# Kernel optimization log

Hardware: AMD Instinct MI355X
Metric: run time of the kernel (lower is better)

Reference implementation:

```python
import jax, jax.numpy as jnp
import numpy as np

B, T, C = 2, 2048, 1024
N_HEADS = 16
HEAD_DIM = C // N_HEADS

def setup_inputs() -> dict:
    key = jax.random.key(0)
    k1, k2, k3 = jax.random.split(key, 3)
    x = jax.random.normal(k1, (B, T, C), dtype=jnp.float32)
    W_qkv = jax.random.normal(k2, (C, 3 * C), dtype=jnp.float32) * (1.0 / np.sqrt(C))
    W_out = jax.random.normal(k3, (C, C), dtype=jnp.float32) * (1.0 / np.sqrt(C))
    return {"x": x, "W_qkv": W_qkv, "W_out": W_out}

def reference(x, W_qkv, W_out):
    b, t, c = x.shape
    qkv = jnp.einsum('btc,cd->btd', x, W_qkv)  # [B,T,3C]
    q, k, v = jnp.split(qkv, 3, axis=-1)
    # [B, H, T, hd]
    q = q.reshape(b, t, N_HEADS, HEAD_DIM).transpose(0, 2, 1, 3)
    k = k.reshape(b, t, N_HEADS, HEAD_DIM).transpose(0, 2, 1, 3)
    v = v.reshape(b, t, N_HEADS, HEAD_DIM).transpose(0, 2, 1, 3)
    scale = 1.0 / jnp.sqrt(jnp.asarray(HEAD_DIM, dtype=x.dtype))
    attn = jnp.einsum('bhqd,bhkd->bhqk', q, k) * scale  # [B,H,T,T]
    causal = jnp.tril(jnp.ones((t, t), dtype=bool))
    attn = jnp.where(causal, attn, jnp.asarray(-1e9, dtype=attn.dtype))
    attn = jax.nn.softmax(attn, axis=-1)
    out = jnp.einsum('bhqk,bhkd->bhqd', attn, v)
    out = out.transpose(0, 2, 1, 3).reshape(b, t, c)
    return jnp.einsum('btc,cd->btd', out, W_out)
```

## Files before the change

### kernel.cpp

```cpp
#include <hip/hip_runtime.h>
#include <hip/hip_bf16.h>

typedef __attribute__((ext_vector_type(8))) short short8;
typedef __attribute__((ext_vector_type(4))) short bf16x4;
typedef __attribute__((ext_vector_type(4))) float floatx4;

#define T_SEQ 2048
#define NH    16
#define HD    64
#define QSCALE 0.18033688f
#define EXP2(x) __builtin_amdgcn_exp2f(x)

#define MFMA16(a, b, c) __builtin_amdgcn_mfma_f32_16x16x16bf16_1k(a, b, c, 0, 0, 0)

__device__ __forceinline__ ushort f2bf(float f) {
    union { float f; unsigned u; } un; un.f = f;
    unsigned r = un.u + 0x7fff + ((un.u >> 16) & 1);
    return (ushort)(r >> 16);
}
__device__ __forceinline__ unsigned pkbf(float a, float b) {
    __hip_bfloat162 t = __float22bfloat162_rn(float2{a, b});
    return *reinterpret_cast<unsigned*>(&t);
}

typedef const __attribute__((address_space(1))) unsigned int* gp1_t;
typedef __attribute__((address_space(3))) unsigned int* lp3_t;
__device__ __forceinline__ void gl_lds16(const ushort* g, ushort* l) {
    __builtin_amdgcn_global_load_lds((gp1_t)g, (lp3_t)l, 16, 0, 0);
}

__global__ void prep_kernel(const float* __restrict__ Wqkv, const float* __restrict__ Wout,
                            const float* __restrict__ x, ushort* __restrict__ wt_qkv,
                            ushort* __restrict__ wt_out, ushort* __restrict__ x_bf) {
    __shared__ ushort tile[32][33];
    const int bid = blockIdx.x;
    if (bid >= 4096) {
        size_t i = ((size_t)(bid - 4096) * 256 + threadIdx.x) * 8;
        float4 f0 = *(const float4*)(x + i);
        float4 f1 = *(const float4*)(x + i + 4);
        short8 v;
        v[0] = (short)f2bf(f0.x); v[1] = (short)f2bf(f0.y);
        v[2] = (short)f2bf(f0.z); v[3] = (short)f2bf(f0.w);
        v[4] = (short)f2bf(f1.x); v[5] = (short)f2bf(f1.y);
        v[6] = (short)f2bf(f1.z); v[7] = (short)f2bf(f1.w);
        *(short8*)(x_bf + i) = v;
        return;
    }
    const float* in; ushort* out; int R, C, gx, gy;
    if (bid < 3072) { in = Wqkv; out = wt_qkv; R = 1024; C = 3072; gx = bid % 96; gy = bid / 96; }
    else            { int t = bid - 3072; in = Wout; out = wt_out; R = 1024; C = 1024; gx = t & 31; gy = t >> 5; }
    const int tx = threadIdx.x & 31, ty = threadIdx.x >> 5;
    const int bx = gx * 32, by = gy * 32;
    #pragma unroll
    for (int i = ty; i < 32; i += 8)
        tile[i][tx] = f2bf(in[(size_t)(by + i) * C + bx + tx]);
    __syncthreads();
    #pragma unroll
    for (int i = ty; i < 32; i += 8)
        out[(size_t)(bx + i) * R + by + tx] = tile[tx][i];
}

template <int EPI>
__global__ __launch_bounds__(256, 3)
void gemm_bt(const ushort* __restrict__ A, const ushort* __restrict__ Bt,
             void* __restrict__ O0, ushort* __restrict__ O1, ushort* __restrict__ O2,
             int M, int N, int K) {
    __shared__ __align__(16) ushort smem[8704];
    ushort* As = smem;
    ushort* Bs = smem + 4096;
    const int tid  = threadIdx.x;
    const int wave = tid >> 6, lane = tid & 63;
    const int quad = lane >> 4, l16 = lane & 15;
    const int wm = (wave >> 1) * 64, wn = (wave & 1) * 64;
    const int m0 = blockIdx.x * 128, n0 = blockIdx.y * 128;

    const int c0 = tid, c1 = tid + 256;
    const int row0 = c0 >> 2, row1 = c1 >> 2;
    const int g0 = (((c0 & 3) ^ ((row0 >> 1) & 3))) * 8;
    const int g1 = (((c1 & 3) ^ ((row1 >> 1) & 3))) * 8;
    const ushort* aP0 = A  + (size_t)(m0 + row0) * K + g0;
    const ushort* aP1 = A  + (size_t)(m0 + row1) * K + g1;
    const ushort* bP0 = Bt + (size_t)(n0 + row0) * K + g0;
    const ushort* bP1 = Bt + (size_t)(n0 + row1) * K + g1;

    floatx4 acc[4][4];
    #pragma unroll
    for (int i = 0; i < 4; i++)
        #pragma unroll
        for (int j = 0; j < 4; j++)
            acc[i][j] = (floatx4){0.f, 0.f, 0.f, 0.f};

    const int col_sw = (quad ^ ((l16 >> 1) & 3)) * 8;

    for (int k0 = 0; k0 < K; k0 += 32) {
        __syncthreads();
        gl_lds16(aP0 + k0, &As[c0 * 8]);
        gl_lds16(aP1 + k0, &As[c1 * 8]);
        gl_lds16(bP0 + k0, &Bs[c0 * 8]);
        gl_lds16(bP1 + k0, &Bs[c1 * 8]);
        __syncthreads();
        short8 af[4], bf[4];
        #pragma unroll
        for (int i = 0; i < 4; i++)
            af[i] = *(const short8*)(&As[(wm + i * 16 + l16) * 32 + col_sw]);
        #pragma unroll
        for (int j = 0; j < 4; j++)
            bf[j] = *(const short8*)(&Bs[(wn + j * 16 + l16) * 32 + col_sw]);
        #pragma unroll
        for (int i = 0; i < 4; i++)
            #pragma unroll
            for (int j = 0; j < 4; j++)
                acc[i][j] = __builtin_amdgcn_mfma_f32_16x16x32_bf16(af[i], bf[j], acc[i][j], 0, 0, 0);
    }

    if (EPI == 0 && n0 >= 2048) {
        const int b = m0 >> 11;
        const int t0 = m0 & 2047;
        const int head0 = (n0 - 2048) >> 6;
        __syncthreads();
        #pragma unroll
        for (int nh = 0; nh < 2; nh++) {
            if ((wave & 1) == nh) {
                #pragma unroll
                for (int j = 0; j < 4; j++)
                    #pragma unroll
                    for (int i = 0; i < 4; i++) {
                        int nl = j * 16 + l16;
                        int mB = wm + i * 16 + quad * 4;
                        *(unsigned*)(&smem[nl * 136 + mB])     = pkbf(acc[i][j][0], acc[i][j][1]);
                        *(unsigned*)(&smem[nl * 136 + mB + 2]) = pkbf(acc[i][j][2], acc[i][j][3]);
                    }
            }
            __syncthreads();
            #pragma unroll
            for (int cc = 0; cc < 4; cc++) {
                int c = cc * 256 + tid;
                int row = c >> 4, mcol = (c & 15) * 8;
                uint4 v = *(const uint4*)(&smem[row * 136 + mcol]);
                *(uint4*)(&O2[((size_t)(b * NH + head0 + nh) * HD + row) * T_SEQ + t0 + mcol]) = v;
            }
            __syncthreads();
        }
        return;
    }

    #pragma unroll
    for (int i = 0; i < 4; i++) {
        #pragma unroll
        for (int j = 0; j < 4; j++) {
            #pragma unroll
            for (int r = 0; r < 4; r++) {
                int m = m0 + wm + i * 16 + quad * 4 + r;
                int n = n0 + wn + j * 16 + l16;
                if (EPI == 0) {
                    int b = m >> 11, t = m & 2047;
                    int part = n >> 10, c = n & 1023;
                    int head = c >> 6, off = c & 63;
                    float av = acc[i][j][r];
                    if (part == 0) av *= QSCALE;
                    ushort v = f2bf(av);
                    if (part == 0) ((ushort*)O0)[(((size_t)(b * NH + head)) * T_SEQ + t) * HD + off] = v;
                    else           O1[(((size_t)(b * NH + head)) * T_SEQ + t) * HD + off] = v;
                } else {
                    ((float*)O0)[(size_t)m * N + n] = acc[i][j][r];
                }
            }
        }
    }
}

__device__ __forceinline__ void softmax_step(floatx4 s[4], float& mst, float& lst,
                                             floatx4 o[4], bf16x4 pf[4]) {
    float t0 = fmaxf(fmaxf(s[0][0], s[0][1]), fmaxf(s[0][2], s[0][3]));
    float t1 = fmaxf(fmaxf(s[1][0], s[1][1]), fmaxf(s[1][2], s[1][3]));
    float t2 = fmaxf(fmaxf(s[2][0], s[2][1]), fmaxf(s[2][2], s[2][3]));
    float t3 = fmaxf(fmaxf(s[3][0], s[3][1]), fmaxf(s[3][2], s[3][3]));
    float t = fmaxf(fmaxf(t0, t1), fmaxf(t2, t3));
    t = fmaxf(t, __shfl_xor(t, 16));
    t = fmaxf(t, __shfl_xor(t, 32));
    const bool nm = t > mst;
    const float mnew = nm ? t : mst;
    float lsum = 0.f;
    #pragma unroll
    for (int j = 0; j < 4; j++) {
        float p0 = EXP2(s[j][0] - mnew);
        float p1 = EXP2(s[j][1] - mnew);
        float p2 = EXP2(s[j][2] - mnew);
        float p3 = EXP2(s[j][3] - mnew);
        lsum += (p0 + p1) + (p2 + p3);
        union { bf16x4 v; unsigned u[2]; } pu;
        pu.u[0] = pkbf(p0, p1);
        pu.u[1] = pkbf(p2, p3);
        pf[j] = pu.v;
    }
    lsum += __shfl_xor(lsum, 16);
    lsum += __shfl_xor(lsum, 32);
    if (__ballot(nm)) {
        float alpha = EXP2(mst - mnew);
        mst = mnew;
        lst = lst * alpha + lsum;
        #pragma unroll
        for (int db = 0; db < 4; db++)
            #pragma unroll
            for (int r = 0; r < 4; r++) o[db][r] *= alpha;
    } else {
        lst += lsum;
    }
}

__global__ __launch_bounds__(256, 5)
void attn_kernel(const ushort* __restrict__ Q, const ushort* __restrict__ Kk,
                 const ushort* __restrict__ Vt, ushort* __restrict__ Oout,
                 float* __restrict__ pm, float* __restrict__ pl, float* __restrict__ po) {
    __shared__ __align__(16) ushort KsA[8192];
    __shared__ __align__(16) ushort VsA[8192];
    const int tid  = threadIdx.x;
    const int wave = tid >> 6, lane = tid & 63;
    const int quad = lane >> 4, l16 = lane & 15;
    const int idx = blockIdx.x;
    const int c = idx >> 5, bh = idx & 31;
    const int b = bh >> 4, h = bh & 15;

    int qt, kb, ke, slot = 0;
    bool partial;
    if (c < 32) {
        const int half = c & 1;
        qt = 31 - (c >> 1);
        const int hi = (qt + 2) >> 1;
        if (half == 0) { kb = 0;  ke = hi - 1; }
        else           { kb = hi; ke = qt;     }
        partial = true;
        slot = (bh * 16 + (qt - 16)) * 2 + half;
    } else {
        qt = 47 - c; kb = 0; ke = qt; partial = false;
    }

    const ushort* qp = Q  + (size_t)bh * T_SEQ * HD;
    const ushort* kp = Kk + (size_t)bh * T_SEQ * HD;
    const ushort* vp = Vt + (size_t)bh * HD * T_SEQ;

    const int q0w = qt * 64 + wave * 16;

    short8 qf[2];
    #pragma unroll
    for (int kbd = 0; kbd < 2; kbd++)
        qf[kbd] = *(const short8*)(qp + (size_t)(q0w + l16) * HD + kbd * 32 + quad * 8);

    floatx4 o[4];
    #pragma unroll
    for (int db = 0; db < 4; db++) o[db] = (floatx4){0.f, 0.f, 0.f, 0.f};
    float mst = -1e30f, lst = 0.f;

    const int c0 = tid, c1 = tid + 256;
    const int r0 = c0 >> 3, r1 = c1 >> 3;
    const int g0 = ((c0 & 7) ^ (r0 & 7)) * 8;
    const int g1 = ((c1 & 7) ^ (r1 & 7)) * 8;
    const size_t koff0 = (size_t)r0 * HD + g0,     koff1 = (size_t)r1 * HD + g1;
    const size_t voff0 = (size_t)r0 * T_SEQ + g0,  voff1 = (size_t)r1 * T_SEQ + g1;

    {
        const size_t kst = (size_t)kb * 64 * HD;
        const int    vst = kb * 64;
        gl_lds16(kp + kst + koff0, &KsA[c0 * 8]);
        gl_lds16(kp + kst + koff1, &KsA[c1 * 8]);
        gl_lds16(vp + vst + voff0, &VsA[c0 * 8]);
        gl_lds16(vp + vst + voff1, &VsA[c1 * 8]);
    }

    const int xsw = (l16 & 7), qh = quad >> 1, ql = quad & 1;
    const int ka0 = l16 * 64 + ((quad ^ xsw) * 8);
    const int ka1 = l16 * 64 + (((4 + quad) ^ xsw) * 8);
    int va[4];
    #pragma unroll
    for (int jj = 0; jj < 4; jj++)
        va[jj] = l16 * 64 + (((2 * jj + qh) ^ xsw) * 8) + ql * 4;

    for (int kt = kb; kt <= ke; ++kt) {
        const int bo = ((kt - kb) & 1) << 12;
        __syncthreads();
        if (kt < ke) {
            const size_t kn = (size_t)(kt + 1) * 64 * HD;
            const int    vn = (kt + 1) * 64;
            const int    bn = bo ^ 4096;
            gl_lds16(kp + kn + koff0, &KsA[bn + c0 * 8]);
            gl_lds16(kp + kn + koff1, &KsA[bn + c1 * 8]);
            gl_lds16(vp + vn + voff0, &VsA[bn + c0 * 8]);
            gl_lds16(vp + vn + voff1, &VsA[bn + c1 * 8]);
        }

        floatx4 s[4];
        #pragma unroll
        for (int jj = 0; jj < 4; jj++) s[jj] = (floatx4){0.f, 0.f, 0.f, 0.f};
        #pragma unroll
        for (int jj = 0; jj < 4; jj++) {
            short8 kf0 = *(const short8*)(&KsA[bo + ka0 + jj * 1024]);
            s[jj] = __builtin_amdgcn_mfma_f32_16x16x32_bf16(kf0, qf[0], s[jj], 0, 0, 0);
        }
        #pragma unroll
        for (int jj = 0; jj < 4; jj++) {
            short8 kf1 = *(const short8*)(&KsA[bo + ka1 + jj * 1024]);
            s[jj] = __builtin_amdgcn_mfma_f32_16x16x32_bf16(kf1, qf[1], s[jj], 0, 0, 0);
        }

        if (kt == qt) {
            #pragma unroll
            for (int jj = 0; jj < 4; jj++)
                #pragma unroll
                for (int rr = 0; rr < 4; rr++) {
                    int key = kt * 64 + jj * 16 + quad * 4 + rr;
                    if (key > q0w + l16) s[jj][rr] = -1e30f;
                }
        }

        bf16x4 pf[4];
        softmax_step(s, mst, lst, o, pf);

        #pragma unroll
        for (int jj = 0; jj < 4; jj++)
            #pragma unroll
            for (int db = 0; db < 4; db++) {
                bf16x4 vf = *(const bf16x4*)(&VsA[bo + va[jj] + db * 1024]);
                o[db] = MFMA16(vf, pf[jj], o[db]);
            }
    }

    if (partial) {
        const int row = wave * 16 + l16;
        if (quad == 0) {
            pm[slot * 64 + row] = mst;
            pl[slot * 64 + row] = lst;
        }
        float* pob = po + (size_t)slot * 4096 + row * 64;
        #pragma unroll
        for (int db = 0; db < 4; db++)
            *(float4*)(pob + db * 16 + quad * 4) =
                (float4){o[db][0], o[db][1], o[db][2], o[db][3]};
    } else {
        const float inv = 1.0f / lst;
        const int t = q0w + l16;
        #pragma unroll
        for (int db = 0; db < 4; db++) {
            union { ushort4 w; unsigned u[2]; } ou;
            ou.u[0] = pkbf(o[db][0] * inv, o[db][1] * inv);
            ou.u[1] = pkbf(o[db][2] * inv, o[db][3] * inv);
            *(ushort4*)(Oout + (((size_t)b * T_SEQ + t) * NH + h) * HD + db * 16 + quad * 4) = ou.w;
        }
    }
}

__global__ void attn_merge(const float* __restrict__ pm, const float* __restrict__ pl,
                           const float* __restrict__ po, ushort* __restrict__ Oout) {
    const int bid = blockIdx.x;
    const int bh = bid >> 4, qidx = bid & 15;
    const int qt = 16 + qidx;
    const int b = bh >> 4, h = bh & 15;
    const int tid = threadIdx.x;
    const int row = tid >> 2, dq = (tid & 3) * 16;
    const int s0 = (bh * 16 + qidx) * 2, s1 = s0 + 1;

    const float m0 = pm[s0 * 64 + row], m1 = pm[s1 * 64 + row];
    const float l0 = pl[s0 * 64 + row], l1 = pl[s1 * 64 + row];
    const float m  = fmaxf(m0, m1);
    const float a0 = EXP2(m0 - m), a1 = EXP2(m1 - m);
    const float inv = 1.0f / (a0 * l0 + a1 * l1);
    const float c0 = a0 * inv, c1 = a1 * inv;

    const float* p0 = po + (size_t)s0 * 4096 + row * 64 + dq;
    const float* p1 = po + (size_t)s1 * 4096 + row * 64 + dq;
    const int t = qt * 64 + row;
    ushort* op = Oout + (((size_t)b * T_SEQ + t) * NH + h) * HD + dq;
    #pragma unroll
    for (int i = 0; i < 4; i++) {
        float4 f0 = *(const float4*)(p0 + i * 4);
        float4 f1 = *(const float4*)(p1 + i * 4);
        union { ushort4 w; unsigned u[2]; } ou;
        ou.u[0] = pkbf(c0 * f0.x + c1 * f1.x, c0 * f0.y + c1 * f1.y);
        ou.u[1] = pkbf(c0 * f0.z + c1 * f1.z, c0 * f0.w + c1 * f1.w);
        *(ushort4*)(op + i * 4) = ou.w;
    }
}

extern "C" void kernel_launch(void* const* d_in, const int* in_sizes, int n_in,
                              void* d_out, int out_size, void* d_ws, size_t ws_size,
                              hipStream_t stream) {
    const float* x    = (const float*)d_in[0];
    const float* Wqkv = (const float*)d_in[1];
    const float* Wout = (const float*)d_in[2];
    ushort* ws = (ushort*)d_ws;

    ushort* wt_qkv = ws;
    ushort* wt_out = wt_qkv + 3072 * 1024;
    ushort* q_ws   = wt_out + 1024 * 1024;
    ushort* k_ws   = q_ws + 4194304;
    ushort* v_t    = k_ws + 4194304;
    ushort* a_out  = v_t + 4194304;
    ushort* x_bf   = a_out + 4194304;
    float*  pm     = (float*)(x_bf + 4194304);
    float*  pl     = pm + 65536;
    float*  po     = pl + 65536;

    prep_kernel<<<dim3(6144), 256, 0, stream>>>(Wqkv, Wout, x, wt_qkv, wt_out, x_bf);

    gemm_bt<0><<<dim3(32, 24), 256, 0, stream>>>(x_bf, wt_qkv, q_ws, k_ws, v_t, 4096, 3072, 1024);

    attn_kernel<<<dim3(1536), 256, 0, stream>>>(q_ws, k_ws, v_t, a_out, pm, pl, po);
    attn_merge<<<dim3(512), 256, 0, stream>>>(pm, pl, po, a_out);

    gemm_bt<1><<<dim3(32, 8), 256, 0, stream>>>(a_out, wt_out, (float*)d_out, nullptr, nullptr,
                                                4096, 1024, 1024);
}
```

Baseline: 189.2 us.

## Use 128-row query tiles with uniform split-K and table-driven block order

The attention kernel now processes 128 query rows per block, 32 per wave, so each K/V tile loaded into LDS is reused for twice as many queries. Every query tile is split into two key ranges. The halves are scheduled through constant lookup tables that balance the causal work, and all outputs go through the merge kernel. The grid shrinks from 1536 to 1024 blocks and occupancy is lowered to 4 blocks per SM to fit the doubled register state. Waves skip key tiles that lie fully above their diagonal. The cost is more registers per thread, fewer resident waves, and a merge pass over every query tile instead of half of them.

```diff
diff --git a/kernel.cpp b/kernel.cpp
--- a/kernel.cpp
+++ b/kernel.cpp
@@ -28,6 +28,15 @@
 __device__ __forceinline__ void gl_lds16(const ushort* g, ushort* l) {
     __builtin_amdgcn_global_load_lds((gp1_t)g, (lp3_t)l, 16, 0, 0);
 }
+
+__constant__ unsigned char PTAB[32] = {15,15,14,14,11,11, 9, 9,
+                                       13,12,13,12,10,10, 8, 8,
+                                        2, 3, 2, 3, 5, 5, 7, 7,
+                                        0, 0, 1, 1, 4, 4, 6, 6};
+__constant__ unsigned char HTAB[32] = {0,1,0,1,0,1,0,1,
+                                       0,0,1,1,0,1,0,1,
+                                       0,0,1,1,0,1,0,1,
+                                       0,1,0,1,0,1,0,1};
 
 __global__ void prep_kernel(const float* __restrict__ Wqkv, const float* __restrict__ Wout,
                             const float* __restrict__ x, ushort* __restrict__ wt_qkv,
@@ -133,8 +142,8 @@
             }
             __syncthreads();
             #pragma unroll
-            for (int cc = 0; cc < 4; cc++) {
-                int c = cc * 256 + tid;
+            for (int cc2 = 0; cc2 < 4; cc2++) {
+                int c = cc2 * 256 + tid;
                 int row = c >> 4, mcol = (c & 15) * 8;
                 uint4 v = *(const uint4*)(&smem[row * 136 + mcol]);
                 *(uint4*)(&O2[((size_t)(b * NH + head0 + nh) * HD + row) * T_SEQ + t0 + mcol]) = v;
@@ -208,9 +217,9 @@
     }
 }
 
-__global__ __launch_bounds__(256, 5)
+__global__ __launch_bounds__(256, 4)
 void attn_kernel(const ushort* __restrict__ Q, const ushort* __restrict__ Kk,
-                 const ushort* __restrict__ Vt, ushort* __restrict__ Oout,
+                 const ushort* __restrict__ Vt,
                  float* __restrict__ pm, float* __restrict__ pl, float* __restrict__ po) {
     __shared__ __align__(16) ushort KsA[8192];
     __shared__ __align__(16) ushort VsA[8192];
@@ -218,38 +227,34 @@
     const int wave = tid >> 6, lane = tid & 63;
     const int quad = lane >> 4, l16 = lane & 15;
     const int idx = blockIdx.x;
-    const int c = idx >> 5, bh = idx & 31;
-    const int b = bh >> 4, h = bh & 15;
-
-    int qt, kb, ke, slot = 0;
-    bool partial;
-    if (c < 32) {
-        const int half = c & 1;
-        qt = 31 - (c >> 1);
-        const int hi = (qt + 2) >> 1;
-        if (half == 0) { kb = 0;  ke = hi - 1; }
-        else           { kb = hi; ke = qt;     }
-        partial = true;
-        slot = (bh * 16 + (qt - 16)) * 2 + half;
-    } else {
-        qt = 47 - c; kb = 0; ke = qt; partial = false;
-    }
+    const int cc = idx >> 5, bh = idx & 31;
+
+    const int p = PTAB[cc], half = HTAB[cc];
+    const int kb = half ? (p + 1) : 0;
+    const int ke = half ? (2 * p + 1) : p;
+    const int slot = (bh * 16 + p) * 2 + half;
 
     const ushort* qp = Q  + (size_t)bh * T_SEQ * HD;
     const ushort* kp = Kk + (size_t)bh * T_SEQ * HD;
     const ushort* vp = Vt + (size_t)bh * HD * T_SEQ;
 
-    const int q0w = qt * 64 + wave * 16;
-
-    short8 qf[2];
-    #pragma unroll
-    for (int kbd = 0; kbd < 2; kbd++)
-        qf[kbd] = *(const short8*)(qp + (size_t)(q0w + l16) * HD + kbd * 32 + quad * 8);
-
-    floatx4 o[4];
-    #pragma unroll
-    for (int db = 0; db < 4; db++) o[db] = (floatx4){0.f, 0.f, 0.f, 0.f};
-    float mst = -1e30f, lst = 0.f;
+    const int q0 = p * 128 + wave * 32;
+
+    short8 qf[2][2];
+    #pragma unroll
+    for (int qi = 0; qi < 2; qi++)
+        #pragma unroll
+        for (int kc = 0; kc < 2; kc++)
+            qf[qi][kc] = *(const short8*)(qp + (size_t)(q0 + qi * 16 + l16) * HD + kc * 32 + quad * 8);
+
+    floatx4 o[2][4];
+    float mst[2], lst[2];
+    #pragma unroll
+    for (int qi = 0; qi < 2; qi++) {
+        #pragma unroll
+        for (int db = 0; db < 4; db++) o[qi][db] = (floatx4){0.f, 0.f, 0.f, 0.f};
+        mst[qi] = -1e30f; lst[qi] = 0.f;
+    }
 
     const int c0 = tid, c1 = tid + 256;
     const int r0 = c0 >> 3, r1 = c1 >> 3;
@@ -288,89 +293,91 @@
             gl_lds16(vp + vn + voff1, &VsA[bn + c1 * 8]);
         }
 
-        floatx4 s[4];
-        #pragma unroll
-        for (int jj = 0; jj < 4; jj++) s[jj] = (floatx4){0.f, 0.f, 0.f, 0.f};
-        #pragma unroll
-        for (int jj = 0; jj < 4; jj++) {
-            short8 kf0 = *(const short8*)(&KsA[bo + ka0 + jj * 1024]);
-            s[jj] = __builtin_amdgcn_mfma_f32_16x16x32_bf16(kf0, qf[0], s[jj], 0, 0, 0);
-        }
-        #pragma unroll
-        for (int jj = 0; jj < 4; jj++) {
-            short8 kf1 = *(const short8*)(&KsA[bo + ka1 + jj * 1024]);
-            s[jj] = __builtin_amdgcn_mfma_f32_16x16x32_bf16(kf1, qf[1], s[jj], 0, 0, 0);
-        }
-
-        if (kt == qt) {
+        const int kw = kt * 64;
+        if (kw <= q0 + 31) {
+            floatx4 s[2][4];
+            #pragma unroll
+            for (int qi = 0; qi < 2; qi++)
+                #pragma unroll
+                for (int jj = 0; jj < 4; jj++) s[qi][jj] = (floatx4){0.f, 0.f, 0.f, 0.f};
+
+            #pragma unroll
+            for (int jj = 0; jj < 4; jj++) {
+                short8 kf0 = *(const short8*)(&KsA[bo + ka0 + jj * 1024]);
+                s[0][jj] = __builtin_amdgcn_mfma_f32_16x16x32_bf16(kf0, qf[0][0], s[0][jj], 0, 0, 0);
+                s[1][jj] = __builtin_amdgcn_mfma_f32_16x16x32_bf16(kf0, qf[1][0], s[1][jj], 0, 0, 0);
+            }
+            #pragma unroll
+            for (int jj = 0; jj < 4; jj++) {
+                short8 kf1 = *(const short8*)(&KsA[bo + ka1 + jj * 1024]);
+                s[0][jj] = __builtin_amdgcn_mfma_f32_16x16x32_bf16(kf1, qf[0][1], s[0][jj], 0, 0, 0);
+                s[1][jj] = __builtin_amdgcn_mfma_f32_16x16x32_bf16(kf1, qf[1][1], s[1][jj], 0, 0, 0);
+            }
+
+            if (kw + 63 > q0) {
+                #pragma unroll
+                for (int qi = 0; qi < 2; qi++)
+                    #pragma unroll
+                    for (int jj = 0; jj < 4; jj++)
+                        #pragma unroll
+                        for (int rr = 0; rr < 4; rr++) {
+                            int key = kw + jj * 16 + quad * 4 + rr;
+                            if (key > q0 + qi * 16 + l16) s[qi][jj][rr] = -1e30f;
+                        }
+            }
+
+            bf16x4 pf[2][4];
+            softmax_step(s[0], mst[0], lst[0], o[0], pf[0]);
+            softmax_step(s[1], mst[1], lst[1], o[1], pf[1]);
+
             #pragma unroll
             for (int jj = 0; jj < 4; jj++)
                 #pragma unroll
-                for (int rr = 0; rr < 4; rr++) {
-                    int key = kt * 64 + jj * 16 + quad * 4 + rr;
-                    if (key > q0w + l16) s[jj][rr] = -1e30f;
+                for (int db = 0; db < 4; db++) {
+                    bf16x4 vf = *(const bf16x4*)(&VsA[bo + va[jj] + db * 1024]);
+                    o[0][db] = MFMA16(vf, pf[0][jj], o[0][db]);
+                    o[1][db] = MFMA16(vf, pf[1][jj], o[1][db]);
                 }
         }
-
-        bf16x4 pf[4];
-        softmax_step(s, mst, lst, o, pf);
-
-        #pragma unroll
-        for (int jj = 0; jj < 4; jj++)
-            #pragma unroll
-            for (int db = 0; db < 4; db++) {
-                bf16x4 vf = *(const bf16x4*)(&VsA[bo + va[jj] + db * 1024]);
-                o[db] = MFMA16(vf, pf[jj], o[db]);
-            }
-    }
-
-    if (partial) {
-        const int row = wave * 16 + l16;
+    }
+
+    #pragma unroll
+    for (int qi = 0; qi < 2; qi++) {
+        const int rowk = wave * 32 + qi * 16 + l16;
         if (quad == 0) {
-            pm[slot * 64 + row] = mst;
-            pl[slot * 64 + row] = lst;
+            pm[slot * 128 + rowk] = mst[qi];
+            pl[slot * 128 + rowk] = lst[qi];
         }
-        float* pob = po + (size_t)slot * 4096 + row * 64;
+        float* pob = po + (size_t)slot * 8192 + rowk * 64;
         #pragma unroll
         for (int db = 0; db < 4; db++)
             *(float4*)(pob + db * 16 + quad * 4) =
-                (float4){o[db][0], o[db][1], o[db][2], o[db][3]};
-    } else {
-        const float inv = 1.0f / lst;
-        const int t = q0w + l16;
-        #pragma unroll
-        for (int db = 0; db < 4; db++) {
-            union { ushort4 w; unsigned u[2]; } ou;
-            ou.u[0] = pkbf(o[db][0] * inv, o[db][1] * inv);
-            ou.u[1] = pkbf(o[db][2] * inv, o[db][3] * inv);
-            *(ushort4*)(Oout + (((size_t)b * T_SEQ + t) * NH + h) * HD + db * 16 + quad * 4) = ou.w;
-        }
+                (float4){o[qi][db][0], o[qi][db][1], o[qi][db][2], o[qi][db][3]};
     }
 }
 
 __global__ void attn_merge(const float* __restrict__ pm, const float* __restrict__ pl,
                            const float* __restrict__ po, ushort* __restrict__ Oout) {
     const int bid = blockIdx.x;
-    const int bh = bid >> 4, qidx = bid & 15;
-    const int qt = 16 + qidx;
+    const int bh = bid >> 4, p = bid & 15;
     const int b = bh >> 4, h = bh & 15;
     const int tid = threadIdx.x;
-    const int row = tid >> 2, dq = (tid & 3) * 16;
-    const int s0 = (bh * 16 + qidx) * 2, s1 = s0 + 1;
-
-    const float m0 = pm[s0 * 64 + row], m1 = pm[s1 * 64 + row];
-    const float l0 = pl[s0 * 64 + row], l1 = pl[s1 * 64 + row];
+    const int rowk = tid >> 1, dh = (tid & 1) * 32;
+    const int s0 = (bh * 16 + p) * 2, s1 = s0 + 1;
+
+    const float m0 = pm[s0 * 128 + rowk], m1 = pm[s1 * 128 + rowk];
+    const float l0 = pl[s0 * 128 + rowk], l1 = pl[s1 * 128 + rowk];
     const float m  = fmaxf(m0, m1);
     const float a0 = EXP2(m0 - m), a1 = EXP2(m1 - m);
     const float inv = 1.0f / (a0 * l0 + a1 * l1);
     const float c0 = a0 * inv, c1 = a1 * inv;
 
-    const float* p0 = po + (size_t)s0 * 4096 + row * 64 + dq;
-    const float* p1 = po + (size_t)s1 * 4096 + row * 64 + dq;
-    const int t = qt * 64 + row;
-    ushort* op = Oout + (((size_t)b * T_SEQ + t) * NH + h) * HD + dq;
-    #pragma unroll
-    for (int i = 0; i < 4; i++) {
+    const float* p0 = po + (size_t)s0 * 8192 + rowk * 64 + dh;
+    const float* p1 = po + (size_t)s1 * 8192 + rowk * 64 + dh;
+    const int t = p * 128 + rowk;
+    ushort* op = Oout + (((size_t)b * T_SEQ + t) * NH + h) * HD + dh;
+    #pragma unroll
+    for (int i = 0; i < 8; i++) {
         float4 f0 = *(const float4*)(p0 + i * 4);
         float4 f1 = *(const float4*)(p1 + i * 4);
         union { ushort4 w; unsigned u[2]; } ou;
@@ -396,14 +403,14 @@
     ushort* a_out  = v_t + 4194304;
     ushort* x_bf   = a_out + 4194304;
     float*  pm     = (float*)(x_bf + 4194304);
-    float*  pl     = pm + 65536;
-    float*  po     = pl + 65536;
+    float*  pl     = pm + 131072;
+    float*  po     = pl + 131072;
 
     prep_kernel<<<dim3(6144), 256, 0, stream>>>(Wqkv, Wout, x, wt_qkv, wt_out, x_bf);
 
     gemm_bt<0><<<dim3(32, 24), 256, 0, stream>>>(x_bf, wt_qkv, q_ws, k_ws, v_t, 4096, 3072, 1024);
 
-    attn_kernel<<<dim3(1536), 256, 0, stream>>>(q_ws, k_ws, v_t, a_out, pm, pl, po);
+    attn_kernel<<<dim3(1024), 256, 0, stream>>>(q_ws, k_ws, v_t, pm, pl, po);
     attn_merge<<<dim3(512), 256, 0, stream>>>(pm, pl, po, a_out);
 
     gemm_bt<1><<<dim3(32, 8), 256, 0, stream>>>(a_out, wt_out, (float*)d_out, nullptr, nullptr,
```

New measurement: 203.4 us. 7.5% more time.
